# Kernel optimization log

Hardware: AMD Instinct MI355X
Metric: run time of the kernel (lower is better)

Reference implementation:

```python
import jax, jax.numpy as jnp
import numpy as np

B, S, D = 4, 2048, 1024
EPS = 1e-6


def setup_inputs() -> dict:
    key = jax.random.key(0)
    ks = jax.random.split(key, 9)
    s = 1.0 / np.sqrt(D)
    return {
        "context": jax.random.normal(ks[0], (B, S, D), jnp.float32),
        "eos_mask": jax.random.randint(ks[1], (B, S, S), 0, 2, dtype=jnp.int32),
        "prior": jax.random.uniform(ks[2], (B, S, S), jnp.float32),
        "Wq": jax.random.uniform(ks[3], (D, D), jnp.float32, -s, s),
        "bq": jax.random.uniform(ks[4], (D,), jnp.float32, -s, s),
        "Wk": jax.random.uniform(ks[5], (D, D), jnp.float32, -s, s),
        "bk": jax.random.uniform(ks[6], (D,), jnp.float32, -s, s),
        "gamma": jnp.ones((D,), jnp.float32),
        "beta": jnp.zeros((D,), jnp.float32),
    }


def reference(context, eos_mask, prior, Wq, bq, Wk, bk, gamma, beta):
    d = context.shape[-1]
    seq = context.shape[1]

    # LayerNorm with torch's unbiased std (Bessel correction)
    mean = jnp.mean(context, axis=-1, keepdims=True)
    var = jnp.sum((context - mean) ** 2, axis=-1, keepdims=True) / (d - 1)
    x = gamma * (context - mean) / (jnp.sqrt(var) + EPS) + beta

    q = x @ Wq + bq  # linear_query
    k = x @ Wk + bk  # linear_key

    scores = jnp.einsum("bid,bjd->bij", q, k) / d  # note: /d, not /sqrt(d)

    idx = jnp.arange(seq)
    band = jnp.abs(idx[:, None] - idx[None, :]) == 1      # a + c (tridiagonal off-diagonals)
    sup = (idx[None, :] - idx[:, None]) == 1              # a (superdiagonal)
    strict_upper = idx[:, None] < idx[None, :]            # triu(ones) - eye
    eye = idx[:, None] == idx[None, :]

    mask = (eos_mask != 0) & band[None]                   # eos_mask & (a + c)
    scores = jnp.where(mask, scores, -1e9)
    na = jax.nn.softmax(scores, axis=-1)
    na = jnp.sqrt(na * jnp.swapaxes(na, -1, -2) + 1e-9)
    na = prior + (1.0 - prior) * na                       # hier_add_index branch

    # t = log(na+eps).masked_fill(a==0,0) @ triu  ==  cumsum along last axis
    t = jnp.where(sup[None], jnp.log(na + 1e-9), 0.0)
    t = jnp.cumsum(t, axis=-1)
    # g = triu @ t  ==  reversed cumsum along axis -2
    g = jnp.cumsum(t[..., ::-1, :], axis=-2)[..., ::-1, :]
    g = jnp.where(strict_upper[None], jnp.exp(g), 0.0)

    g_attn = g + jnp.swapaxes(g, -1, -2) + jnp.where(eye[None], na, 1e-9)
    return (g_attn, na)
```

## Files before the change

kernel.cpp:

```cpp
#include <hip/hip_runtime.h>
#include <hip/hip_bf16.h>
#include <cmath>

#define BB 4
#define SS 2048
#define DD 1024
#define BS (BB*SS)
constexpr float EPS = 1e-6f;

typedef __attribute__((ext_vector_type(8))) short short8;
typedef __attribute__((ext_vector_type(4))) float floatx4;

__global__ __launch_bounds__(256)
void wconv_kernel(const float* __restrict__ Wq, const float* __restrict__ Wk,
                  __hip_bfloat16* __restrict__ Wb) {
    int idx = blockIdx.x * 256 + threadIdx.x;
    const int half = DD * DD / 4;
    const float* src = (idx < half) ? Wk : Wq;
    int off = (idx < half) ? idx : idx - half;
    float4 v = ((const float4*)src)[off];
    union { ushort4 u; __hip_bfloat16 h[4]; } pk;
    pk.h[0] = __float2bfloat16(v.x);
    pk.h[1] = __float2bfloat16(v.y);
    pk.h[2] = __float2bfloat16(v.z);
    pk.h[3] = __float2bfloat16(v.w);
    ((ushort4*)Wb)[idx] = pk.u;
}

__global__ __launch_bounds__(256)
void gemv_kernel(const float* __restrict__ Wq, const float* __restrict__ Wk,
                 const float* __restrict__ bq, const float* __restrict__ bk,
                 float* __restrict__ u, float* __restrict__ v, float* __restrict__ cs) {
    int gid = blockIdx.x * 4 + (threadIdx.x >> 6);
    int lane = threadIdx.x & 63;
    if (gid > 2048) return;
    const float* row; const float* vec; float* outp;
    if (gid < 1024)      { row = Wq + (size_t)gid * DD;          vec = bk; outp = u + gid; }
    else if (gid < 2048) { row = Wk + (size_t)(gid - 1024) * DD; vec = bq; outp = v + (gid - 1024); }
    else                 { row = bq;                             vec = bk; outp = cs; }
    float s = 0.f;
    #pragma unroll
    for (int k = 0; k < 4; ++k) {
        float4 a = ((const float4*)row)[lane * 4 + k];
        float4 b = ((const float4*)vec)[lane * 4 + k];
        s += a.x * b.x + a.y * b.y + a.z * b.z + a.w * b.w;
    }
    #pragma unroll
    for (int off = 32; off; off >>= 1) s += __shfl_down(s, off);
    if (lane == 0) *outp = s;
}

__global__ __launch_bounds__(256)
void ln_kernel(const float* __restrict__ ctx, const float* __restrict__ gamma,
               const float* __restrict__ beta, const float* __restrict__ u,
               const float* __restrict__ v, const float* __restrict__ cs,
               __hip_bfloat16* __restrict__ xo, float* __restrict__ alpha,
               float* __restrict__ betav) {
    int row = blockIdx.x;
    int t = threadIdx.x;
    const float* r = ctx + (size_t)row * DD;
    float4 val = ((const float4*)r)[t];
    float s1 = val.x + val.y + val.z + val.w;
    float s2 = val.x*val.x + val.y*val.y + val.z*val.z + val.w*val.w;
    #pragma unroll
    for (int off = 32; off; off >>= 1) {
        s1 += __shfl_down(s1, off);
        s2 += __shfl_down(s2, off);
    }
    __shared__ float ls1[4], ls2[4];
    int wid = t >> 6, lane = t & 63;
    if (lane == 0) { ls1[wid] = s1; ls2[wid] = s2; }
    __syncthreads();
    if (t == 0) {
        float a = ls1[0] + ls1[1] + ls1[2] + ls1[3];
        float b = ls2[0] + ls2[1] + ls2[2] + ls2[3];
        float mean = a / DD;
        float var = (b - a * a / DD) / (DD - 1);
        ls1[0] = mean;
        ls2[0] = 1.0f / (sqrtf(var) + EPS);
    }
    __syncthreads();
    float mean = ls1[0], rstd = ls2[0];
    float4 g = ((const float4*)gamma)[t];
    float4 be = ((const float4*)beta)[t];
    float nx0 = g.x * (val.x - mean) * rstd + be.x;
    float nx1 = g.y * (val.y - mean) * rstd + be.y;
    float nx2 = g.z * (val.z - mean) * rstd + be.z;
    float nx3 = g.w * (val.w - mean) * rstd + be.w;
    union { ushort4 uu; __hip_bfloat16 h[4]; } pk;
    pk.h[0] = __float2bfloat16(nx0);
    pk.h[1] = __float2bfloat16(nx1);
    pk.h[2] = __float2bfloat16(nx2);
    pk.h[3] = __float2bfloat16(nx3);
    ((ushort4*)(xo + (size_t)row * DD))[t] = pk.uu;
    float4 u4 = ((const float4*)u)[t];
    float4 v4 = ((const float4*)v)[t];
    float du = nx0 * u4.x + nx1 * u4.y + nx2 * u4.z + nx3 * u4.w;
    float dv = nx0 * v4.x + nx1 * v4.y + nx2 * v4.z + nx3 * v4.w;
    #pragma unroll
    for (int off = 32; off; off >>= 1) {
        du += __shfl_down(du, off);
        dv += __shfl_down(dv, off);
    }
    __syncthreads();
    if (lane == 0) { ls1[wid] = du; ls2[wid] = dv; }
    __syncthreads();
    if (t == 0) {
        alpha[row] = ls1[0] + ls1[1] + ls1[2] + ls1[3] + *cs;
        betav[row] = ls2[0] + ls2[1] + ls2[2] + ls2[3];
    }
}

#define TM 128
#define TN 128
#define TK 32
__global__ __launch_bounds__(256)
void gemm_mfma(const __hip_bfloat16* __restrict__ A,
               const __hip_bfloat16* __restrict__ B,
               __hip_bfloat16* __restrict__ C, int ldc) {
    __shared__ short smem[18432];
    short* As = smem;
    short* Bs = smem + TM * TK;
    int tid = threadIdx.x;
    int wave = tid >> 6;
    int lane = tid & 63;
    int wm = wave >> 1, wn = wave & 1;
    int q = lane >> 4, m16 = lane & 15;

    int srow = lane >> 2;
    int skoff = (lane & 3) * 8;
    const __hip_bfloat16* gA = A + ((size_t)blockIdx.x * TM + wave * 32 + srow) * DD + skoff;
    const __hip_bfloat16* gB = B + ((size_t)blockIdx.y * TN + wave * 32 + srow) * DD + skoff;
    short* lAbase = As + (wave * 32) * TK;
    short* lBbase = Bs + (wave * 32) * TK;

    floatx4 acc[4][4] = {};

    for (int k0 = 0; k0 < DD; k0 += TK) {
        __builtin_amdgcn_global_load_lds(
            (const __attribute__((address_space(1))) void*)(gA + k0),
            (__attribute__((address_space(3))) void*)(lAbase), 16, 0, 0);
        __builtin_amdgcn_global_load_lds(
            (const __attribute__((address_space(1))) void*)(gA + k0 + 16 * DD),
            (__attribute__((address_space(3))) void*)(lAbase + 16 * TK), 16, 0, 0);
        __builtin_amdgcn_global_load_lds(
            (const __attribute__((address_space(1))) void*)(gB + k0),
            (__attribute__((address_space(3))) void*)(lBbase), 16, 0, 0);
        __builtin_amdgcn_global_load_lds(
            (const __attribute__((address_space(1))) void*)(gB + k0 + 16 * DD),
            (__attribute__((address_space(3))) void*)(lBbase + 16 * TK), 16, 0, 0);
        __syncthreads();
        short8 af[4], bf[4];
        #pragma unroll
        for (int r = 0; r < 4; ++r)
            af[r] = *(const short8*)(As + (wm * 64 + r * 16 + m16) * TK + q * 8);
        #pragma unroll
        for (int c = 0; c < 4; ++c)
            bf[c] = *(const short8*)(Bs + (wn * 64 + c * 16 + m16) * TK + q * 8);
        #pragma unroll
        for (int r = 0; r < 4; ++r)
            #pragma unroll
            for (int c = 0; c < 4; ++c)
                acc[r][c] = __builtin_amdgcn_mfma_f32_16x16x32_bf16(af[r], bf[c], acc[r][c], 0, 0, 0);
        __syncthreads();
    }

    short* EP = smem + wave * 4608;
    #pragma unroll
    for (int r = 0; r < 4; ++r)
        #pragma unroll
        for (int c = 0; c < 4; ++c)
            #pragma unroll
            for (int e = 0; e < 4; ++e) {
                __hip_bfloat16 hv = __float2bfloat16(acc[r][c][e]);
                EP[(r * 16 + q * 4 + e) * 72 + c * 16 + m16] = *(short*)&hv;
            }
    int grow0 = blockIdx.x * TM + wm * 64;
    int gcol0 = blockIdx.y * TN + wn * 64;
    short* Cc = (short*)C;
    #pragma unroll
    for (int it = 0; it < 8; ++it) {
        int rl = it * 8 + (lane >> 3);
        int cg = (lane & 7) * 8;
        short8 vv = *(const short8*)(EP + rl * 72 + cg);
        *(short8*)(Cc + (size_t)(grow0 + rl) * ldc + gcol0 + cg) = vv;
    }
}

__global__ __launch_bounds__(256)
void band_kernel(const __hip_bfloat16* __restrict__ z, const __hip_bfloat16* __restrict__ x,
                 const int* __restrict__ eos, const float* __restrict__ alpha,
                 const float* __restrict__ betav, float* __restrict__ vsub,
                 float* __restrict__ vsup, float* __restrict__ wuni) {
    int gw = (blockIdx.x * blockDim.x + threadIdx.x) >> 6;
    int lane = threadIdx.x & 63;
    int i = gw & (SS - 1);
    float zv[16];
    {
        const ushort4* p = (const ushort4*)(z + (size_t)gw * DD + lane * 16);
        #pragma unroll
        for (int m = 0; m < 4; ++m) {
            union { ushort4 u; __hip_bfloat16 h[4]; } cv; cv.u = p[m];
            #pragma unroll
            for (int r = 0; r < 4; ++r) zv[m * 4 + r] = __bfloat162float(cv.h[r]);
        }
    }
    float ssup = 0.f, ssub = 0.f;
    if (i < SS - 1) {
        const ushort4* p = (const ushort4*)(x + (size_t)(gw + 1) * DD + lane * 16);
        #pragma unroll
        for (int m = 0; m < 4; ++m) {
            union { ushort4 u; __hip_bfloat16 h[4]; } cv; cv.u = p[m];
            #pragma unroll
            for (int r = 0; r < 4; ++r) ssup += zv[m * 4 + r] * __bfloat162float(cv.h[r]);
        }
    }
    if (i > 0) {
        const ushort4* p = (const ushort4*)(x + (size_t)(gw - 1) * DD + lane * 16);
        #pragma unroll
        for (int m = 0; m < 4; ++m) {
            union { ushort4 u; __hip_bfloat16 h[4]; } cv; cv.u = p[m];
            #pragma unroll
            for (int r = 0; r < 4; ++r) ssub += zv[m * 4 + r] * __bfloat162float(cv.h[r]);
        }
    }
    #pragma unroll
    for (int off = 32; off; off >>= 1) {
        ssup += __shfl_down(ssup, off);
        ssub += __shfl_down(ssub, off);
    }
    if (lane == 0) {
        float a = alpha[gw];
        if (i < SS - 1) ssup = (ssup + a + betav[gw + 1]) * (1.0f / DD);
        if (i > 0)      ssub = (ssub + a + betav[gw - 1]) * (1.0f / DD);
        bool msub = (i > 0) && (eos[(size_t)gw * SS + (i - 1)] != 0);
        bool msup = (i < SS - 1) && (eos[(size_t)gw * SS + (i + 1)] != 0);
        float vs, vp, w;
        if (msub && msup) {
            float mx = fmaxf(ssub, ssup);
            float e1 = expf(ssub - mx), e2 = expf(ssup - mx);
            float inv = 1.0f / (e1 + e2);
            vs = e1 * inv; vp = e2 * inv; w = 0.f;
        } else if (msub) { vs = 1.f; vp = 0.f; w = 0.f; }
        else if (msup)   { vs = 0.f; vp = 1.f; w = 0.f; }
        else             { vs = vp = w = 1.0f / SS; }
        vsub[gw] = vs; vsup[gw] = vp; wuni[gw] = w;
    }
}

__global__ __launch_bounds__(256)
void scan_kernel(const float* __restrict__ prior, const float* __restrict__ vsub,
                 const float* __restrict__ vsup, double* __restrict__ Lc) {
    int b = blockIdx.x;
    int t = threadIdx.x;
    double loc[8];
    double s = 0.0;
    #pragma unroll
    for (int k = 0; k < 8; ++k) {
        int tt = t * 8 + k;
        double Lv = 0.0;
        if (tt < SS - 1) {
            float pr = prior[((size_t)(b * SS + tt)) * SS + tt + 1];
            float na2 = sqrtf(vsup[b * SS + tt] * vsub[b * SS + tt + 1] + 1e-9f);
            float P = pr + (1.f - pr) * na2;
            Lv = log((double)P + 1e-9);
        }
        loc[k] = Lv; s += Lv;
    }
    __shared__ double sa[256], sb[256];
    sa[t] = s;
    __syncthreads();
    double* src = sa; double* dst = sb;
    for (int off = 1; off < 256; off <<= 1) {
        double v = src[t];
        if (t >= off) v += src[t - off];
        __syncthreads();
        dst[t] = v;
        __syncthreads();
        double* tmp = src; src = dst; dst = tmp;
    }
    double run = (t == 0) ? 0.0 : src[t - 1];
    #pragma unroll
    for (int k = 0; k < 8; ++k) {
        int idx = t * 8 + k;
        Lc[b * SS + idx] = run;
        run += loc[k];
    }
}

__global__ __launch_bounds__(256)
void out_kernel(const float* __restrict__ prior, const float* __restrict__ vsub,
                const float* __restrict__ vsup, const float* __restrict__ wuni,
                const double* __restrict__ Lc, float* __restrict__ out_g,
                float* __restrict__ out_na) {
    size_t gid = (size_t)blockIdx.x * 256 + threadIdx.x;
    int jt = (int)(gid & 511);
    int row = (int)(gid >> 9);
    int i = row & (SS - 1);
    int b = row >> 11;
    int j0 = jt * 4;
    size_t base = (size_t)row * SS + j0;
    float4 pr4 = *(const float4*)(prior + base);
    float4 wj4 = *(const float4*)(wuni + b * SS + j0);
    float pra[4] = {pr4.x, pr4.y, pr4.z, pr4.w};
    float wja[4] = {wj4.x, wj4.y, wj4.z, wj4.w};
    float wi = wuni[row];
    double Lci = Lc[row];
    const double* Lcb = Lc + b * SS;
    float nav[4], gv[4];
    #pragma unroll
    for (int c = 0; c < 4; ++c) {
        int j = j0 + c;
        float prod;
        if (j == i - 1)      prod = vsub[row] * vsup[row - 1];
        else if (j == i + 1) prod = vsup[row] * vsub[row + 1];
        else if (j == i)     prod = wi * wi;
        else                 prod = wi * wja[c];
        float na2 = sqrtf(prod + 1e-9f);
        float p = pra[c];
        float na3 = p + (1.f - p) * na2;
        nav[c] = na3;
        if (j == i) {
            gv[c] = na3;
        } else {
            double d = (j > i) ? (Lcb[j] - Lci) : (Lci - Lcb[j]);
            gv[c] = expf((float)d) + 1e-9f;
        }
    }
    *(float4*)(out_g + base) = make_float4(gv[0], gv[1], gv[2], gv[3]);
    *(float4*)(out_na + base) = make_float4(nav[0], nav[1], nav[2], nav[3]);
}

extern "C" void kernel_launch(void* const* d_in, const int* in_sizes, int n_in,
                              void* d_out, int out_size, void* d_ws, size_t ws_size,
                              hipStream_t stream) {
    const float* ctx   = (const float*)d_in[0];
    const int*   eos   = (const int*)d_in[1];
    const float* prior = (const float*)d_in[2];
    const float* Wq    = (const float*)d_in[3];
    const float* bq    = (const float*)d_in[4];
    const float* Wk    = (const float*)d_in[5];
    const float* bk    = (const float*)d_in[6];
    const float* gamma = (const float*)d_in[7];
    const float* beta  = (const float*)d_in[8];

    float* out_g  = (float*)d_out;
    float* out_na = out_g + (size_t)BB * SS * SS;

    char* ws = (char*)d_ws;
    size_t o = 0;
    __hip_bfloat16* x  = (__hip_bfloat16*)(ws + o); o += (size_t)BS * DD * 2;
    __hip_bfloat16* z  = (__hip_bfloat16*)(ws + o); o += (size_t)BS * DD * 2;
    __hip_bfloat16* Wb = (__hip_bfloat16*)(ws + o); o += (size_t)2 * DD * DD * 2;
    __hip_bfloat16* Mt = (__hip_bfloat16*)(ws + o); o += (size_t)DD * DD * 2;
    double* Lc   = (double*)(ws + o); o += (size_t)BS * 8;
    float* u     = (float*)(ws + o);  o += DD * 4;
    float* v     = (float*)(ws + o);  o += DD * 4;
    float* cs    = (float*)(ws + o);  o += 64;
    float* alpha = (float*)(ws + o);  o += (size_t)BS * 4;
    float* betav = (float*)(ws + o);  o += (size_t)BS * 4;
    float* vsub  = (float*)(ws + o);  o += (size_t)BS * 4;
    float* vsup  = (float*)(ws + o);  o += (size_t)BS * 4;
    float* wuni  = (float*)(ws + o);  o += (size_t)BS * 4;

    __hip_bfloat16* Wk_bf = Wb;
    __hip_bfloat16* Wq_bf = Wb + (size_t)DD * DD;

    wconv_kernel<<<(2 * DD * DD / 4) / 256, 256, 0, stream>>>(Wq, Wk, Wb);
    gemv_kernel<<<513, 256, 0, stream>>>(Wq, Wk, bq, bk, u, v, cs);
    ln_kernel<<<BS, 256, 0, stream>>>(ctx, gamma, beta, u, v, cs, x, alpha, betav);

    dim3 g1(DD / TM, DD / TN);
    gemm_mfma<<<g1, 256, 0, stream>>>(Wk_bf, Wq_bf, Mt, DD);

    dim3 g2(BS / TM, DD / TN);
    gemm_mfma<<<g2, 256, 0, stream>>>(x, Mt, z, DD);

    band_kernel<<<BS / 4, 256, 0, stream>>>(z, x, eos, alpha, betav, vsub, vsup, wuni);

    scan_kernel<<<BB, 256, 0, stream>>>(prior, vsub, vsup, Lc);

    size_t total = (size_t)BB * SS * SS / 4;
    out_kernel<<<(int)(total / 256), 256, 0, stream>>>(prior, vsub, vsup, wuni, Lc,
                                                       out_g, out_na);
}
```

Measured before the change: 337.4 us.

## Fuse band dot-products into GEMM epilogue, merge prep kernels, smaller tiles for weight GEMM

The second GEMM no longer writes the full bf16 z matrix. Its epilogue computes the partial dot products of each z row with the neighbouring x rows and accumulates them into a small buffer with atomics, and a light softmax kernel then finishes the band logic. The weight-conversion, GEMV and accumulator-zeroing steps are merged into one launch, and the Wk·Wq GEMM switches to 64x64 tiles to get more blocks. This removes a 16MB write and re-read of z and a few launches, at the cost of float atomics, whose summation order is nondeterministic, and higher register pressure in the epilogue.

```diff
diff --git a/kernel.cpp b/kernel.cpp
--- a/kernel.cpp
+++ b/kernel.cpp
@@ -11,43 +11,53 @@
 typedef __attribute__((ext_vector_type(8))) short short8;
 typedef __attribute__((ext_vector_type(4))) float floatx4;
 
-__global__ __launch_bounds__(256)
-void wconv_kernel(const float* __restrict__ Wq, const float* __restrict__ Wk,
-                  __hip_bfloat16* __restrict__ Wb) {
-    int idx = blockIdx.x * 256 + threadIdx.x;
-    const int half = DD * DD / 4;
-    const float* src = (idx < half) ? Wk : Wq;
-    int off = (idx < half) ? idx : idx - half;
-    float4 v = ((const float4*)src)[off];
-    union { ushort4 u; __hip_bfloat16 h[4]; } pk;
-    pk.h[0] = __float2bfloat16(v.x);
-    pk.h[1] = __float2bfloat16(v.y);
-    pk.h[2] = __float2bfloat16(v.z);
-    pk.h[3] = __float2bfloat16(v.w);
-    ((ushort4*)Wb)[idx] = pk.u;
-}
-
-__global__ __launch_bounds__(256)
-void gemv_kernel(const float* __restrict__ Wq, const float* __restrict__ Wk,
+__device__ inline float bf2f(unsigned short u) {
+    unsigned v = ((unsigned)u) << 16;
+    float f; __builtin_memcpy(&f, &v, 4);
+    return f;
+}
+
+__global__ __launch_bounds__(256)
+void prep_kernel(const float* __restrict__ Wq, const float* __restrict__ Wk,
                  const float* __restrict__ bq, const float* __restrict__ bk,
-                 float* __restrict__ u, float* __restrict__ v, float* __restrict__ cs) {
-    int gid = blockIdx.x * 4 + (threadIdx.x >> 6);
-    int lane = threadIdx.x & 63;
-    if (gid > 2048) return;
-    const float* row; const float* vec; float* outp;
-    if (gid < 1024)      { row = Wq + (size_t)gid * DD;          vec = bk; outp = u + gid; }
-    else if (gid < 2048) { row = Wk + (size_t)(gid - 1024) * DD; vec = bq; outp = v + (gid - 1024); }
-    else                 { row = bq;                             vec = bk; outp = cs; }
-    float s = 0.f;
-    #pragma unroll
-    for (int k = 0; k < 4; ++k) {
-        float4 a = ((const float4*)row)[lane * 4 + k];
-        float4 b = ((const float4*)vec)[lane * 4 + k];
-        s += a.x * b.x + a.y * b.y + a.z * b.z + a.w * b.w;
-    }
-    #pragma unroll
-    for (int off = 32; off; off >>= 1) s += __shfl_down(s, off);
-    if (lane == 0) *outp = s;
+                 __hip_bfloat16* __restrict__ Wb, float* __restrict__ u,
+                 float* __restrict__ v, float* __restrict__ cs,
+                 float* __restrict__ sacc) {
+    int blk = blockIdx.x;
+    if (blk < 2048) {
+        int idx = blk * 256 + threadIdx.x;
+        const int half = DD * DD / 4;
+        const float* src = (idx < half) ? Wk : Wq;
+        int off = (idx < half) ? idx : idx - half;
+        float4 val = ((const float4*)src)[off];
+        union { ushort4 uu; __hip_bfloat16 h[4]; } pk;
+        pk.h[0] = __float2bfloat16(val.x);
+        pk.h[1] = __float2bfloat16(val.y);
+        pk.h[2] = __float2bfloat16(val.z);
+        pk.h[3] = __float2bfloat16(val.w);
+        ((ushort4*)Wb)[idx] = pk.uu;
+    } else if (blk < 2561) {
+        int gid = (blk - 2048) * 4 + (threadIdx.x >> 6);
+        int lane = threadIdx.x & 63;
+        if (gid > 2048) return;
+        const float* row; const float* vec; float* outp;
+        if (gid < 1024)      { row = Wq + (size_t)gid * DD;          vec = bk; outp = u + gid; }
+        else if (gid < 2048) { row = Wk + (size_t)(gid - 1024) * DD; vec = bq; outp = v + (gid - 1024); }
+        else                 { row = bq;                             vec = bk; outp = cs; }
+        float s = 0.f;
+        #pragma unroll
+        for (int k = 0; k < 4; ++k) {
+            float4 a = ((const float4*)row)[lane * 4 + k];
+            float4 b = ((const float4*)vec)[lane * 4 + k];
+            s += a.x * b.x + a.y * b.y + a.z * b.z + a.w * b.w;
+        }
+        #pragma unroll
+        for (int off = 32; off; off >>= 1) s += __shfl_down(s, off);
+        if (lane == 0) *outp = s;
+    } else {
+        int idx = (blk - 2561) * 1024 + threadIdx.x * 4;
+        *(float4*)(sacc + idx) = make_float4(0.f, 0.f, 0.f, 0.f);
+    }
 }
 
 __global__ __launch_bounds__(256)
@@ -111,13 +121,70 @@
     }
 }
 
+__global__ __launch_bounds__(256)
+void gemm64_mfma(const __hip_bfloat16* __restrict__ A,
+                 const __hip_bfloat16* __restrict__ B,
+                 __hip_bfloat16* __restrict__ C, int ldc) {
+    __shared__ short As[64 * 64];
+    __shared__ short Bs[64 * 64];
+    int tid = threadIdx.x;
+    int wave = tid >> 6;
+    int lane = tid & 63;
+    int q = lane >> 4, m16 = lane & 15;
+    int srow = lane >> 3;
+    int skoff = (lane & 7) * 8;
+
+    const __hip_bfloat16* gA = A + ((size_t)blockIdx.x * 64 + wave * 16 + srow) * DD + skoff;
+    const __hip_bfloat16* gB = B + ((size_t)blockIdx.y * 64 + wave * 16 + srow) * DD + skoff;
+    short* lA0 = As + (wave * 16) * 64;
+    short* lA1 = As + (wave * 16 + 8) * 64;
+    short* lB0 = Bs + (wave * 16) * 64;
+    short* lB1 = Bs + (wave * 16 + 8) * 64;
+
+    floatx4 acc[4] = {};
+    for (int k0 = 0; k0 < DD; k0 += 64) {
+        __builtin_amdgcn_global_load_lds(
+            (const __attribute__((address_space(1))) void*)(gA + k0),
+            (__attribute__((address_space(3))) void*)(lA0), 16, 0, 0);
+        __builtin_amdgcn_global_load_lds(
+            (const __attribute__((address_space(1))) void*)(gA + k0 + 8 * DD),
+            (__attribute__((address_space(3))) void*)(lA1), 16, 0, 0);
+        __builtin_amdgcn_global_load_lds(
+            (const __attribute__((address_space(1))) void*)(gB + k0),
+            (__attribute__((address_space(3))) void*)(lB0), 16, 0, 0);
+        __builtin_amdgcn_global_load_lds(
+            (const __attribute__((address_space(1))) void*)(gB + k0 + 8 * DD),
+            (__attribute__((address_space(3))) void*)(lB1), 16, 0, 0);
+        __syncthreads();
+        #pragma unroll
+        for (int h = 0; h < 2; ++h) {
+            short8 af = *(const short8*)(As + (wave * 16 + m16) * 64 + h * 32 + q * 8);
+            #pragma unroll
+            for (int c = 0; c < 4; ++c) {
+                short8 bf_ = *(const short8*)(Bs + (c * 16 + m16) * 64 + h * 32 + q * 8);
+                acc[c] = __builtin_amdgcn_mfma_f32_16x16x32_bf16(af, bf_, acc[c], 0, 0, 0);
+            }
+        }
+        __syncthreads();
+    }
+    #pragma unroll
+    for (int c = 0; c < 4; ++c) {
+        int gcol = blockIdx.y * 64 + c * 16 + m16;
+        #pragma unroll
+        for (int e = 0; e < 4; ++e) {
+            int grow = blockIdx.x * 64 + wave * 16 + q * 4 + e;
+            C[(size_t)grow * ldc + gcol] = __float2bfloat16(acc[c][e]);
+        }
+    }
+}
+
 #define TM 128
 #define TN 128
 #define TK 32
 __global__ __launch_bounds__(256)
-void gemm_mfma(const __hip_bfloat16* __restrict__ A,
-               const __hip_bfloat16* __restrict__ B,
-               __hip_bfloat16* __restrict__ C, int ldc) {
+void gemm2_fused(const __hip_bfloat16* __restrict__ A,
+                 const __hip_bfloat16* __restrict__ B,
+                 float* __restrict__ sacc) {
     __shared__ short smem[18432];
     short* As = smem;
     short* Bs = smem + TM * TK;
@@ -150,18 +217,18 @@
             (const __attribute__((address_space(1))) void*)(gB + k0 + 16 * DD),
             (__attribute__((address_space(3))) void*)(lBbase + 16 * TK), 16, 0, 0);
         __syncthreads();
-        short8 af[4], bf[4];
+        short8 af[4], bf_[4];
         #pragma unroll
         for (int r = 0; r < 4; ++r)
             af[r] = *(const short8*)(As + (wm * 64 + r * 16 + m16) * TK + q * 8);
         #pragma unroll
         for (int c = 0; c < 4; ++c)
-            bf[c] = *(const short8*)(Bs + (wn * 64 + c * 16 + m16) * TK + q * 8);
+            bf_[c] = *(const short8*)(Bs + (wn * 64 + c * 16 + m16) * TK + q * 8);
         #pragma unroll
         for (int r = 0; r < 4; ++r)
             #pragma unroll
             for (int c = 0; c < 4; ++c)
-                acc[r][c] = __builtin_amdgcn_mfma_f32_16x16x32_bf16(af[r], bf[c], acc[r][c], 0, 0, 0);
+                acc[r][c] = __builtin_amdgcn_mfma_f32_16x16x32_bf16(af[r], bf_[c], acc[r][c], 0, 0, 0);
         __syncthreads();
     }
 
@@ -175,77 +242,64 @@
                 __hip_bfloat16 hv = __float2bfloat16(acc[r][c][e]);
                 EP[(r * 16 + q * 4 + e) * 72 + c * 16 + m16] = *(short*)&hv;
             }
-    int grow0 = blockIdx.x * TM + wm * 64;
+
+    int rl = lane;
+    int growZ = blockIdx.x * TM + wm * 64 + rl;
     int gcol0 = blockIdx.y * TN + wn * 64;
-    short* Cc = (short*)C;
-    #pragma unroll
-    for (int it = 0; it < 8; ++it) {
-        int rl = it * 8 + (lane >> 3);
-        int cg = (lane & 7) * 8;
-        short8 vv = *(const short8*)(EP + rl * 72 + cg);
-        *(short8*)(Cc + (size_t)(grow0 + rl) * ldc + gcol0 + cg) = vv;
-    }
-}
-
-__global__ __launch_bounds__(256)
-void band_kernel(const __hip_bfloat16* __restrict__ z, const __hip_bfloat16* __restrict__ x,
-                 const int* __restrict__ eos, const float* __restrict__ alpha,
-                 const float* __restrict__ betav, float* __restrict__ vsub,
-                 float* __restrict__ vsup, float* __restrict__ wuni) {
-    int gw = (blockIdx.x * blockDim.x + threadIdx.x) >> 6;
-    int lane = threadIdx.x & 63;
+    float zf[64];
+    #pragma unroll
+    for (int c8 = 0; c8 < 8; ++c8) {
+        short8 zz = *(const short8*)(EP + rl * 72 + c8 * 8);
+        #pragma unroll
+        for (int e = 0; e < 8; ++e) zf[c8 * 8 + e] = bf2f((unsigned short)zz[e]);
+    }
+    if (growZ + 1 < BS) {
+        const short8* px = (const short8*)(A + (size_t)(growZ + 1) * DD + gcol0);
+        float sup = 0.f;
+        #pragma unroll
+        for (int c8 = 0; c8 < 8; ++c8) {
+            short8 xx = px[c8];
+            #pragma unroll
+            for (int e = 0; e < 8; ++e) sup += zf[c8 * 8 + e] * bf2f((unsigned short)xx[e]);
+        }
+        atomicAdd(&sacc[growZ], sup);
+    }
+    if (growZ >= 1) {
+        const short8* px = (const short8*)(A + (size_t)(growZ - 1) * DD + gcol0);
+        float sub = 0.f;
+        #pragma unroll
+        for (int c8 = 0; c8 < 8; ++c8) {
+            short8 xx = px[c8];
+            #pragma unroll
+            for (int e = 0; e < 8; ++e) sub += zf[c8 * 8 + e] * bf2f((unsigned short)xx[e]);
+        }
+        atomicAdd(&sacc[BS + growZ], sub);
+    }
+}
+
+__global__ __launch_bounds__(256)
+void softmax_kernel(const float* __restrict__ sacc, const int* __restrict__ eos,
+                    const float* __restrict__ alpha, const float* __restrict__ betav,
+                    float* __restrict__ vsub, float* __restrict__ vsup,
+                    float* __restrict__ wuni) {
+    int gw = blockIdx.x * 256 + threadIdx.x;
     int i = gw & (SS - 1);
-    float zv[16];
-    {
-        const ushort4* p = (const ushort4*)(z + (size_t)gw * DD + lane * 16);
-        #pragma unroll
-        for (int m = 0; m < 4; ++m) {
-            union { ushort4 u; __hip_bfloat16 h[4]; } cv; cv.u = p[m];
-            #pragma unroll
-            for (int r = 0; r < 4; ++r) zv[m * 4 + r] = __bfloat162float(cv.h[r]);
-        }
-    }
+    float a = alpha[gw];
     float ssup = 0.f, ssub = 0.f;
-    if (i < SS - 1) {
-        const ushort4* p = (const ushort4*)(x + (size_t)(gw + 1) * DD + lane * 16);
-        #pragma unroll
-        for (int m = 0; m < 4; ++m) {
-            union { ushort4 u; __hip_bfloat16 h[4]; } cv; cv.u = p[m];
-            #pragma unroll
-            for (int r = 0; r < 4; ++r) ssup += zv[m * 4 + r] * __bfloat162float(cv.h[r]);
-        }
-    }
-    if (i > 0) {
-        const ushort4* p = (const ushort4*)(x + (size_t)(gw - 1) * DD + lane * 16);
-        #pragma unroll
-        for (int m = 0; m < 4; ++m) {
-            union { ushort4 u; __hip_bfloat16 h[4]; } cv; cv.u = p[m];
-            #pragma unroll
-            for (int r = 0; r < 4; ++r) ssub += zv[m * 4 + r] * __bfloat162float(cv.h[r]);
-        }
-    }
-    #pragma unroll
-    for (int off = 32; off; off >>= 1) {
-        ssup += __shfl_down(ssup, off);
-        ssub += __shfl_down(ssub, off);
-    }
-    if (lane == 0) {
-        float a = alpha[gw];
-        if (i < SS - 1) ssup = (ssup + a + betav[gw + 1]) * (1.0f / DD);
-        if (i > 0)      ssub = (ssub + a + betav[gw - 1]) * (1.0f / DD);
-        bool msub = (i > 0) && (eos[(size_t)gw * SS + (i - 1)] != 0);
-        bool msup = (i < SS - 1) && (eos[(size_t)gw * SS + (i + 1)] != 0);
-        float vs, vp, w;
-        if (msub && msup) {
-            float mx = fmaxf(ssub, ssup);
-            float e1 = expf(ssub - mx), e2 = expf(ssup - mx);
-            float inv = 1.0f / (e1 + e2);
-            vs = e1 * inv; vp = e2 * inv; w = 0.f;
-        } else if (msub) { vs = 1.f; vp = 0.f; w = 0.f; }
-        else if (msup)   { vs = 0.f; vp = 1.f; w = 0.f; }
-        else             { vs = vp = w = 1.0f / SS; }
-        vsub[gw] = vs; vsup[gw] = vp; wuni[gw] = w;
-    }
+    if (i < SS - 1) ssup = (sacc[gw] + a + betav[gw + 1]) * (1.0f / DD);
+    if (i > 0)      ssub = (sacc[BS + gw] + a + betav[gw - 1]) * (1.0f / DD);
+    bool msub = (i > 0) && (eos[(size_t)gw * SS + (i - 1)] != 0);
+    bool msup = (i < SS - 1) && (eos[(size_t)gw * SS + (i + 1)] != 0);
+    float vs, vp, w;
+    if (msub && msup) {
+        float mx = fmaxf(ssub, ssup);
+        float e1 = expf(ssub - mx), e2 = expf(ssup - mx);
+        float inv = 1.0f / (e1 + e2);
+        vs = e1 * inv; vp = e2 * inv; w = 0.f;
+    } else if (msub) { vs = 1.f; vp = 0.f; w = 0.f; }
+    else if (msup)   { vs = 0.f; vp = 1.f; w = 0.f; }
+    else             { vs = vp = w = 1.0f / SS; }
+    vsub[gw] = vs; vsup[gw] = vp; wuni[gw] = w;
 }
 
 __global__ __launch_bounds__(256)
@@ -350,7 +404,6 @@
     char* ws = (char*)d_ws;
     size_t o = 0;
     __hip_bfloat16* x  = (__hip_bfloat16*)(ws + o); o += (size_t)BS * DD * 2;
-    __hip_bfloat16* z  = (__hip_bfloat16*)(ws + o); o += (size_t)BS * DD * 2;
     __hip_bfloat16* Wb = (__hip_bfloat16*)(ws + o); o += (size_t)2 * DD * DD * 2;
     __hip_bfloat16* Mt = (__hip_bfloat16*)(ws + o); o += (size_t)DD * DD * 2;
     double* Lc   = (double*)(ws + o); o += (size_t)BS * 8;
@@ -362,21 +415,21 @@
     float* vsub  = (float*)(ws + o);  o += (size_t)BS * 4;
     float* vsup  = (float*)(ws + o);  o += (size_t)BS * 4;
     float* wuni  = (float*)(ws + o);  o += (size_t)BS * 4;
+    float* sacc  = (float*)(ws + o);  o += (size_t)2 * BS * 4;
 
     __hip_bfloat16* Wk_bf = Wb;
     __hip_bfloat16* Wq_bf = Wb + (size_t)DD * DD;
 
-    wconv_kernel<<<(2 * DD * DD / 4) / 256, 256, 0, stream>>>(Wq, Wk, Wb);
-    gemv_kernel<<<513, 256, 0, stream>>>(Wq, Wk, bq, bk, u, v, cs);
+    prep_kernel<<<2577, 256, 0, stream>>>(Wq, Wk, bq, bk, Wb, u, v, cs, sacc);
     ln_kernel<<<BS, 256, 0, stream>>>(ctx, gamma, beta, u, v, cs, x, alpha, betav);
 
-    dim3 g1(DD / TM, DD / TN);
-    gemm_mfma<<<g1, 256, 0, stream>>>(Wk_bf, Wq_bf, Mt, DD);
+    dim3 g1(DD / 64, DD / 64);
+    gemm64_mfma<<<g1, 256, 0, stream>>>(Wk_bf, Wq_bf, Mt, DD);
 
     dim3 g2(BS / TM, DD / TN);
-    gemm_mfma<<<g2, 256, 0, stream>>>(x, Mt, z, DD);
-
-    band_kernel<<<BS / 4, 256, 0, stream>>>(z, x, eos, alpha, betav, vsub, vsup, wuni);
+    gemm2_fused<<<g2, 256, 0, stream>>>(x, Mt, sacc);
+
+    softmax_kernel<<<BS / 256, 256, 0, stream>>>(sacc, eos, alpha, betav, vsub, vsup, wuni);
 
     scan_kernel<<<BB, 256, 0, stream>>>(prior, vsub, vsup, Lc);
 
```

New measurement: 326.7 us. 3.2% less time.
